# Performance work log

Hardware: AMD Instinct MI355X
Metric: run time of the kernel (lower is better)

Reference implementation:

```python
import jax, jax.numpy as jnp
import numpy as np

LN_EPS = 1e-5


def setup_inputs() -> dict:
    key = jax.random.key(0)
    k1, k2, k3 = jax.random.split(key, 3)
    B, K, S, H, D = 8, 32, 4096, 2048, 1024
    plan_embeddings = jax.random.normal(k1, (B, S, H), dtype=jnp.float32)
    ownership = jax.random.bernoulli(k2, 0.5, (B, K, S))  # bool (B, K, S)
    W = jax.random.normal(k3, (H, D), dtype=jnp.float32) * (1.0 / np.sqrt(H))
    b = jnp.zeros((D,), dtype=jnp.float32)
    gamma = jnp.ones((D,), dtype=jnp.float32)
    beta = jnp.zeros((D,), dtype=jnp.float32)
    return {
        "plan_embeddings": plan_embeddings,
        "ownership": ownership,
        "W": W,
        "b": b,
        "gamma": gamma,
        "beta": beta,
    }


def reference(plan_embeddings, ownership, W, b, gamma, beta):
    # ownership-weighted mean pooling over slots S (same math as the
    # broadcast-multiply + sum in the torch original, expressed as an einsum
    # so no (B,K,S,H) intermediate is materialized)
    own_f = ownership.astype(plan_embeddings.dtype)          # (B, K, S)
    summed = jnp.einsum('bks,bsh->bkh', own_f, plan_embeddings)  # (B, K, H)
    counts = jnp.clip(own_f.sum(axis=-1, keepdims=True), 1.0)   # (B, K, 1)
    pooled = summed / counts                                   # (B, K, H)
    # linear projection
    projected = pooled @ W + b                                 # (B, K, D)
    # LayerNorm over last dim
    mu = projected.mean(axis=-1, keepdims=True)
    var = jnp.mean(jnp.square(projected - mu), axis=-1, keepdims=True)
    normed = (projected - mu) * jax.lax.rsqrt(var + LN_EPS)
    return normed * gamma + beta
```

## Files before the change

kernel.cpp:

```cpp
#include <hip/hip_runtime.h>

typedef unsigned int u32;
typedef unsigned short u16;
typedef __attribute__((ext_vector_type(8))) short short8;
typedef __attribute__((ext_vector_type(4))) float f32x4;

#define BB 8
#define KK 32
#define SS 4096
#define HH 2048
#define DD 1024
#define NSC 8
#define SC_S 512
#define NSLAB 16

#define OFF_W16  0ull
#define OFF_WB   (2ull << 20)
#define OFF_PART (6ull << 20)
#define OFF_PQ   (22ull << 20)
#define OFF_PROJ (23ull << 20)

__device__ __forceinline__ u16 f2bf(float x) {
  u32 u = __float_as_uint(x);
  return (u16)((u + 0x7fffu + ((u >> 16) & 1u)) >> 16);
}

__global__ __launch_bounds__(256) void k_weights(const void* __restrict__ own,
                                                 u16* __restrict__ w16) {
  const int bk = blockIdx.x;
  const int t = threadIdx.x;
  __shared__ int s_mode;
  __shared__ int s_wcnt[4];
  __shared__ float s_inv;

  if (t < 64) {
    u32 w = ((const u32*)own)[t];
    bool wordok = (w <= 1u) || (w == 0x3f800000u);
    unsigned long long m = __ballot(wordok);
    if (t == 0) s_mode = (m == ~0ull) ? 1 : 0;
  }
  __syncthreads();
  const int mode = s_mode;

  u32 bits = 0;
  const size_t base = (size_t)bk * SS + (size_t)t * 16;
  if (mode == 0) {
    uint4 v = *(const uint4*)((const unsigned char*)own + base);
    u32 wa[4] = {v.x, v.y, v.z, v.w};
#pragma unroll
    for (int w = 0; w < 4; ++w)
#pragma unroll
      for (int j = 0; j < 4; ++j)
        if ((wa[w] >> (8 * j)) & 0xffu) bits |= 1u << (4 * w + j);
  } else {
    const u32* p = (const u32*)own + base;
#pragma unroll
    for (int j = 0; j < 16; ++j)
      if (p[j] != 0u) bits |= 1u << j;
  }

  int cnt = __popc(bits);
#pragma unroll
  for (int off = 1; off < 64; off <<= 1) cnt += __shfl_xor(cnt, off);
  if ((t & 63) == 0) s_wcnt[t >> 6] = cnt;
  __syncthreads();
  if (t == 0) {
    int tot = s_wcnt[0] + s_wcnt[1] + s_wcnt[2] + s_wcnt[3];
    s_inv = 1.0f / fmaxf((float)tot, 1.0f);
  }
  __syncthreads();
  const u32 hv = (u32)f2bf(s_inv);

  u32 outw[8];
#pragma unroll
  for (int j = 0; j < 8; ++j) {
    u32 lo = ((bits >> (2 * j)) & 1u) ? hv : 0u;
    u32 hi = ((bits >> (2 * j + 1)) & 1u) ? hv : 0u;
    outw[j] = lo | (hi << 16);
  }
  u32* wo = (u32*)w16 + (size_t)bk * (SS / 2) + (size_t)t * 8;
  uint4 o0 = {outw[0], outw[1], outw[2], outw[3]};
  uint4 o1 = {outw[4], outw[5], outw[6], outw[7]};
  ((uint4*)wo)[0] = o0;
  ((uint4*)wo)[1] = o1;
}

__global__ __launch_bounds__(256) void k_wpackT(const float* __restrict__ W,
                                                u16* __restrict__ WB) {
  __shared__ float lds[64][65];
  const int hb = blockIdx.x * 64, db = blockIdx.y * 64;
  const int x = threadIdx.x & 63, y = threadIdx.x >> 6;
#pragma unroll
  for (int j = 0; j < 16; ++j) {
    int r = y + 4 * j;
    lds[r][x] = W[(size_t)(hb + r) * DD + db + x];
  }
  __syncthreads();
#pragma unroll
  for (int j = 0; j < 16; ++j) {
    int r = y + 4 * j;
    WB[(size_t)(db + r) * HH + hb + x] = f2bf(lds[x][r]);
  }
}

__global__ __launch_bounds__(256) void k_pool(const float* __restrict__ plan,
                                              const u16* __restrict__ w16,
                                              float* __restrict__ part) {
  const int hcl = blockIdx.x, sc = blockIdx.y, b = blockIdx.z;
  const int t = threadIdx.x, w = t >> 6, l = t & 63;
  const int lr = l & 15, lg = l >> 4;
  const int h0 = hcl * 128 + w * 32;
  const int s0 = sc * SC_S;

  const float* pb = plan + (size_t)b * SS * HH;
  f32x4 acc[2][2];
#pragma unroll
  for (int a = 0; a < 2; ++a)
#pragma unroll
    for (int c = 0; c < 2; ++c) acc[a][c] = (f32x4){0.f, 0.f, 0.f, 0.f};

  for (int slab = 0; slab < NSLAB; ++slab) {
    const int sbase = s0 + slab * 32 + lg * 8;
    short8 a0 = *(const short8*)(w16 + ((size_t)(b * KK + lr) * SS + sbase));
    short8 a1 = *(const short8*)(w16 + ((size_t)(b * KK + 16 + lr) * SS + sbase));
#pragma unroll
    for (int tt = 0; tt < 2; ++tt) {
      const float* col = pb + (size_t)sbase * HH + h0 + tt * 16 + lr;
      float f[8];
#pragma unroll
      for (int j = 0; j < 8; ++j) f[j] = col[(size_t)j * HH];
      short8 bfr;
#pragma unroll
      for (int j = 0; j < 8; ++j) bfr[j] = (short)f2bf(f[j]);
      acc[tt][0] = __builtin_amdgcn_mfma_f32_16x16x32_bf16(a0, bfr, acc[tt][0], 0, 0, 0);
      acc[tt][1] = __builtin_amdgcn_mfma_f32_16x16x32_bf16(a1, bfr, acc[tt][1], 0, 0, 0);
    }
  }

  float* po = part + ((size_t)sc * BB + b) * KK * HH;
#pragma unroll
  for (int tt = 0; tt < 2; ++tt)
#pragma unroll
    for (int kt = 0; kt < 2; ++kt)
#pragma unroll
      for (int j = 0; j < 4; ++j) {
        int krow = kt * 16 + lg * 4 + j;
        int hcol = h0 + tt * 16 + lr;
        po[(size_t)krow * HH + hcol] = acc[tt][kt][j];
      }
}

__global__ __launch_bounds__(256) void k_reduce(const float* __restrict__ part,
                                                u32* __restrict__ pq) {
  const int i = blockIdx.x * 256 + threadIdx.x;
  const int row = i >> 10, hp = i & 1023;
  const float* p = part + (size_t)row * HH + 2 * hp;
  float lo = 0.f, hi = 0.f;
#pragma unroll
  for (int sc = 0; sc < NSC; ++sc) {
    float2 v = *(const float2*)(p + (size_t)sc * BB * KK * HH);
    lo += v.x;
    hi += v.y;
  }
  pq[i] = (u32)f2bf(lo) | ((u32)f2bf(hi) << 16);
}

__global__ __launch_bounds__(256) void k_proj(const u16* __restrict__ pq,
                                              const u16* __restrict__ WB,
                                              const float* __restrict__ bias,
                                              float* __restrict__ proj) {
  const int rt = blockIdx.x, ctg = blockIdx.y;
  const int t = threadIdx.x, w = t >> 6, l = t & 63;
  const int lr = l & 15, lg = l >> 4;
  const int r0 = rt * 16, c0 = (ctg * 4 + w) * 16;

  const u16* pa = pq + (size_t)(r0 + lr) * HH + lg * 8;
  const u16* pw = WB + (size_t)(c0 + lr) * HH + lg * 8;
  f32x4 acc = (f32x4){0.f, 0.f, 0.f, 0.f};
#pragma unroll 4
  for (int slab = 0; slab < 64; ++slab) {
    short8 a = *(const short8*)(pa + slab * 32);
    short8 bv = *(const short8*)(pw + slab * 32);
    acc = __builtin_amdgcn_mfma_f32_16x16x32_bf16(a, bv, acc, 0, 0, 0);
  }
  const float bs = bias[c0 + lr];
#pragma unroll
  for (int j = 0; j < 4; ++j)
    proj[(size_t)(r0 + lg * 4 + j) * DD + c0 + lr] = acc[j] + bs;
}

__global__ __launch_bounds__(256) void k_ln(const float* __restrict__ proj,
                                            const float* __restrict__ gamma,
                                            const float* __restrict__ beta,
                                            float* __restrict__ out) {
  const int row = blockIdx.x, t = threadIdx.x;
  float4 v = ((const float4*)(proj + (size_t)row * DD))[t];
  float s1 = v.x + v.y + v.z + v.w;
  float s2 = v.x * v.x + v.y * v.y + v.z * v.z + v.w * v.w;
#pragma unroll
  for (int off = 1; off < 64; off <<= 1) {
    s1 += __shfl_xor(s1, off);
    s2 += __shfl_xor(s2, off);
  }
  __shared__ float a1[4], a2[4];
  if ((t & 63) == 0) { a1[t >> 6] = s1; a2[t >> 6] = s2; }
  __syncthreads();
  const float S1 = a1[0] + a1[1] + a1[2] + a1[3];
  const float S2 = a2[0] + a2[1] + a2[2] + a2[3];
  const float mu = S1 * (1.0f / DD);
  const float var = S2 * (1.0f / DD) - mu * mu;
  const float rs = rsqrtf(var + 1e-5f);
  float4 g = ((const float4*)gamma)[t];
  float4 be = ((const float4*)beta)[t];
  float4 o;
  o.x = (v.x - mu) * rs * g.x + be.x;
  o.y = (v.y - mu) * rs * g.y + be.y;
  o.z = (v.z - mu) * rs * g.z + be.z;
  o.w = (v.w - mu) * rs * g.w + be.w;
  ((float4*)(out + (size_t)row * DD))[t] = o;
}


extern "C" void kernel_launch(void* const* d_in, const int* in_sizes, int n_in,
                              void* d_out, int out_size, void* d_ws, size_t ws_size,
                              hipStream_t stream) {
  (void)in_sizes; (void)n_in; (void)out_size; (void)ws_size;
  const float* plan  = (const float*)d_in[0];
  const void*  own   = d_in[1];
  const float* W     = (const float*)d_in[2];
  const float* bias  = (const float*)d_in[3];
  const float* gamma = (const float*)d_in[4];
  const float* beta  = (const float*)d_in[5];
  float* out = (float*)d_out;
  char* ws = (char*)d_ws;

  u16*   w16  = (u16*)(ws + OFF_W16);
  u16*   WB   = (u16*)(ws + OFF_WB);
  float* part = (float*)(ws + OFF_PART);
  u32*   pq   = (u32*)(ws + OFF_PQ);
  float* proj = (float*)(ws + OFF_PROJ);

  k_weights<<<dim3(BB * KK), dim3(256), 0, stream>>>(own, w16);
  k_wpackT<<<dim3(HH / 64, DD / 64), dim3(256), 0, stream>>>(W, WB);
  k_pool<<<dim3(16, NSC, BB), dim3(256), 0, stream>>>(plan, w16, part);
  k_reduce<<<dim3((BB * KK * (HH / 2)) / 256), dim3(256), 0, stream>>>(part, pq);
  k_proj<<<dim3(16, 16), dim3(256), 0, stream>>>((const u16*)pq, WB, bias, proj);
  k_ln<<<dim3(BB * KK), dim3(256), 0, stream>>>(proj, gamma, beta, out);
}
```

Before: 100.2 us.

## Merge prep kernels and switch pooling to 32x32x16 MFMA tiles

Fuses the ownership-weight kernel and the W transpose/pack kernel into a single launch, with the block index choosing the role. The pooling kernel now uses one 32x32x16 bf16 MFMA per wave covering all 32 K rows and 32 H columns, instead of four 16x16x32 MFMAs. Each plan element is now loaded and converted once per wave, where before it was reused across two K halves, and the inner loop takes twice as many steps. The intent is to cut one launch and reduce MFMA issue count and redundant weight loads. Per-wave load granularity for plan is narrower (32 columns), which may change coalescing.

```diff
diff --git a/kernel.cpp b/kernel.cpp
--- a/kernel.cpp
+++ b/kernel.cpp
@@ -4,6 +4,7 @@
 typedef unsigned short u16;
 typedef __attribute__((ext_vector_type(8))) short short8;
 typedef __attribute__((ext_vector_type(4))) float f32x4;
+typedef __attribute__((ext_vector_type(16))) float f32x16;
 
 #define BB 8
 #define KK 32
@@ -12,7 +13,7 @@
 #define DD 1024
 #define NSC 8
 #define SC_S 512
-#define NSLAB 16
+#define KSTEPS 32
 
 #define OFF_W16  0ull
 #define OFF_WB   (2ull << 20)
@@ -25,81 +26,84 @@
   return (u16)((u + 0x7fffu + ((u >> 16) & 1u)) >> 16);
 }
 
-__global__ __launch_bounds__(256) void k_weights(const void* __restrict__ own,
-                                                 u16* __restrict__ w16) {
-  const int bk = blockIdx.x;
+__global__ __launch_bounds__(256) void k_prep(const void* __restrict__ own,
+                                              u16* __restrict__ w16,
+                                              const float* __restrict__ W,
+                                              u16* __restrict__ WB) {
+  __shared__ float lds[64][65];
   const int t = threadIdx.x;
-  __shared__ int s_mode;
-  __shared__ int s_wcnt[4];
-  __shared__ float s_inv;
-
-  if (t < 64) {
-    u32 w = ((const u32*)own)[t];
-    bool wordok = (w <= 1u) || (w == 0x3f800000u);
-    unsigned long long m = __ballot(wordok);
-    if (t == 0) s_mode = (m == ~0ull) ? 1 : 0;
-  }
-  __syncthreads();
-  const int mode = s_mode;
-
-  u32 bits = 0;
-  const size_t base = (size_t)bk * SS + (size_t)t * 16;
-  if (mode == 0) {
-    uint4 v = *(const uint4*)((const unsigned char*)own + base);
-    u32 wa[4] = {v.x, v.y, v.z, v.w};
-#pragma unroll
-    for (int w = 0; w < 4; ++w)
-#pragma unroll
-      for (int j = 0; j < 4; ++j)
-        if ((wa[w] >> (8 * j)) & 0xffu) bits |= 1u << (4 * w + j);
+
+  if (blockIdx.x < BB * KK) {
+    const int bk = blockIdx.x;
+    __shared__ int s_mode;
+    __shared__ int s_wcnt[4];
+    __shared__ float s_inv;
+
+    if (t < 64) {
+      u32 w = ((const u32*)own)[t];
+      bool wordok = (w <= 1u) || (w == 0x3f800000u);
+      unsigned long long m = __ballot(wordok);
+      if (t == 0) s_mode = (m == ~0ull) ? 1 : 0;
+    }
+    __syncthreads();
+    const int mode = s_mode;
+
+    u32 bits = 0;
+    const size_t base = (size_t)bk * SS + (size_t)t * 16;
+    if (mode == 0) {
+      uint4 v = *(const uint4*)((const unsigned char*)own + base);
+      u32 wa[4] = {v.x, v.y, v.z, v.w};
+#pragma unroll
+      for (int w = 0; w < 4; ++w)
+#pragma unroll
+        for (int j = 0; j < 4; ++j)
+          if ((wa[w] >> (8 * j)) & 0xffu) bits |= 1u << (4 * w + j);
+    } else {
+      const u32* p = (const u32*)own + base;
+#pragma unroll
+      for (int j = 0; j < 16; ++j)
+        if (p[j] != 0u) bits |= 1u << j;
+    }
+
+    int cnt = __popc(bits);
+#pragma unroll
+    for (int off = 1; off < 64; off <<= 1) cnt += __shfl_xor(cnt, off);
+    if ((t & 63) == 0) s_wcnt[t >> 6] = cnt;
+    __syncthreads();
+    if (t == 0) {
+      int tot = s_wcnt[0] + s_wcnt[1] + s_wcnt[2] + s_wcnt[3];
+      s_inv = 1.0f / fmaxf((float)tot, 1.0f);
+    }
+    __syncthreads();
+    const u32 hv = (u32)f2bf(s_inv);
+
+    u32 outw[8];
+#pragma unroll
+    for (int j = 0; j < 8; ++j) {
+      u32 lo = ((bits >> (2 * j)) & 1u) ? hv : 0u;
+      u32 hi = ((bits >> (2 * j + 1)) & 1u) ? hv : 0u;
+      outw[j] = lo | (hi << 16);
+    }
+    u32* wo = (u32*)w16 + (size_t)bk * (SS / 2) + (size_t)t * 8;
+    uint4 o0 = {outw[0], outw[1], outw[2], outw[3]};
+    uint4 o1 = {outw[4], outw[5], outw[6], outw[7]};
+    ((uint4*)wo)[0] = o0;
+    ((uint4*)wo)[1] = o1;
   } else {
-    const u32* p = (const u32*)own + base;
-#pragma unroll
-    for (int j = 0; j < 16; ++j)
-      if (p[j] != 0u) bits |= 1u << j;
-  }
-
-  int cnt = __popc(bits);
-#pragma unroll
-  for (int off = 1; off < 64; off <<= 1) cnt += __shfl_xor(cnt, off);
-  if ((t & 63) == 0) s_wcnt[t >> 6] = cnt;
-  __syncthreads();
-  if (t == 0) {
-    int tot = s_wcnt[0] + s_wcnt[1] + s_wcnt[2] + s_wcnt[3];
-    s_inv = 1.0f / fmaxf((float)tot, 1.0f);
-  }
-  __syncthreads();
-  const u32 hv = (u32)f2bf(s_inv);
-
-  u32 outw[8];
-#pragma unroll
-  for (int j = 0; j < 8; ++j) {
-    u32 lo = ((bits >> (2 * j)) & 1u) ? hv : 0u;
-    u32 hi = ((bits >> (2 * j + 1)) & 1u) ? hv : 0u;
-    outw[j] = lo | (hi << 16);
-  }
-  u32* wo = (u32*)w16 + (size_t)bk * (SS / 2) + (size_t)t * 8;
-  uint4 o0 = {outw[0], outw[1], outw[2], outw[3]};
-  uint4 o1 = {outw[4], outw[5], outw[6], outw[7]};
-  ((uint4*)wo)[0] = o0;
-  ((uint4*)wo)[1] = o1;
-}
-
-__global__ __launch_bounds__(256) void k_wpackT(const float* __restrict__ W,
-                                                u16* __restrict__ WB) {
-  __shared__ float lds[64][65];
-  const int hb = blockIdx.x * 64, db = blockIdx.y * 64;
-  const int x = threadIdx.x & 63, y = threadIdx.x >> 6;
-#pragma unroll
-  for (int j = 0; j < 16; ++j) {
-    int r = y + 4 * j;
-    lds[r][x] = W[(size_t)(hb + r) * DD + db + x];
-  }
-  __syncthreads();
-#pragma unroll
-  for (int j = 0; j < 16; ++j) {
-    int r = y + 4 * j;
-    WB[(size_t)(db + r) * HH + hb + x] = f2bf(lds[x][r]);
+    const int bidx = blockIdx.x - BB * KK;
+    const int hb = (bidx & 31) * 64, db = (bidx >> 5) * 64;
+    const int x = t & 63, y = t >> 6;
+#pragma unroll
+    for (int j = 0; j < 16; ++j) {
+      int r = y + 4 * j;
+      lds[r][x] = W[(size_t)(hb + r) * DD + db + x];
+    }
+    __syncthreads();
+#pragma unroll
+    for (int j = 0; j < 16; ++j) {
+      int r = y + 4 * j;
+      WB[(size_t)(db + r) * HH + hb + x] = f2bf(lds[x][r]);
+    }
   }
 }
 
@@ -108,46 +112,36 @@
                                               float* __restrict__ part) {
   const int hcl = blockIdx.x, sc = blockIdx.y, b = blockIdx.z;
   const int t = threadIdx.x, w = t >> 6, l = t & 63;
-  const int lr = l & 15, lg = l >> 4;
+  const int lc = l & 31, half = l >> 5;
   const int h0 = hcl * 128 + w * 32;
   const int s0 = sc * SC_S;
 
-  const float* pb = plan + (size_t)b * SS * HH;
-  f32x4 acc[2][2];
-#pragma unroll
-  for (int a = 0; a < 2; ++a)
-#pragma unroll
-    for (int c = 0; c < 2; ++c) acc[a][c] = (f32x4){0.f, 0.f, 0.f, 0.f};
-
-  for (int slab = 0; slab < NSLAB; ++slab) {
-    const int sbase = s0 + slab * 32 + lg * 8;
-    short8 a0 = *(const short8*)(w16 + ((size_t)(b * KK + lr) * SS + sbase));
-    short8 a1 = *(const short8*)(w16 + ((size_t)(b * KK + 16 + lr) * SS + sbase));
-#pragma unroll
-    for (int tt = 0; tt < 2; ++tt) {
-      const float* col = pb + (size_t)sbase * HH + h0 + tt * 16 + lr;
-      float f[8];
-#pragma unroll
-      for (int j = 0; j < 8; ++j) f[j] = col[(size_t)j * HH];
-      short8 bfr;
-#pragma unroll
-      for (int j = 0; j < 8; ++j) bfr[j] = (short)f2bf(f[j]);
-      acc[tt][0] = __builtin_amdgcn_mfma_f32_16x16x32_bf16(a0, bfr, acc[tt][0], 0, 0, 0);
-      acc[tt][1] = __builtin_amdgcn_mfma_f32_16x16x32_bf16(a1, bfr, acc[tt][1], 0, 0, 0);
-    }
-  }
-
-  float* po = part + ((size_t)sc * BB + b) * KK * HH;
-#pragma unroll
-  for (int tt = 0; tt < 2; ++tt)
-#pragma unroll
-    for (int kt = 0; kt < 2; ++kt)
-#pragma unroll
-      for (int j = 0; j < 4; ++j) {
-        int krow = kt * 16 + lg * 4 + j;
-        int hcol = h0 + tt * 16 + lr;
-        po[(size_t)krow * HH + hcol] = acc[tt][kt][j];
-      }
+  const float* pb = plan + (size_t)b * SS * HH + h0 + lc;
+  const u16* wa = w16 + (size_t)(b * KK + lc) * SS;
+
+  f32x16 acc;
+#pragma unroll
+  for (int r = 0; r < 16; ++r) acc[r] = 0.0f;
+
+  for (int step = 0; step < KSTEPS; ++step) {
+    const int sb = s0 + step * 16 + half * 8;
+    short8 a = *(const short8*)(wa + sb);
+    const float* col = pb + (size_t)sb * HH;
+    float f[8];
+#pragma unroll
+    for (int j = 0; j < 8; ++j) f[j] = col[(size_t)j * HH];
+    short8 bfr;
+#pragma unroll
+    for (int j = 0; j < 8; ++j) bfr[j] = (short)f2bf(f[j]);
+    acc = __builtin_amdgcn_mfma_f32_32x32x16_bf16(a, bfr, acc, 0, 0, 0);
+  }
+
+  float* po = part + ((size_t)sc * BB + b) * KK * HH + h0 + lc;
+#pragma unroll
+  for (int r = 0; r < 16; ++r) {
+    int krow = (r & 3) + 8 * (r >> 2) + 4 * half;
+    po[(size_t)krow * HH] = acc[r];
+  }
 }
 
 __global__ __launch_bounds__(256) void k_reduce(const float* __restrict__ part,
@@ -240,8 +234,7 @@
   u32*   pq   = (u32*)(ws + OFF_PQ);
   float* proj = (float*)(ws + OFF_PROJ);
 
-  k_weights<<<dim3(BB * KK), dim3(256), 0, stream>>>(own, w16);
-  k_wpackT<<<dim3(HH / 64, DD / 64), dim3(256), 0, stream>>>(W, WB);
+  k_prep<<<dim3(BB * KK + (HH / 64) * (DD / 64)), dim3(256), 0, stream>>>(own, w16, W, WB);
   k_pool<<<dim3(16, NSC, BB), dim3(256), 0, stream>>>(plan, w16, part);
   k_reduce<<<dim3((BB * KK * (HH / 2)) / 256), dim3(256), 0, stream>>>(part, pq);
   k_proj<<<dim3(16, 16), dim3(256), 0, stream>>>((const u16*)pq, WB, bias, proj);
```

Measured after the change: 87.89 us. -12.2%, faster.
